# Performance work log

Measured on AMD Instinct MI355X. Metric: run time of the kernel, lower is better.

## Reference

```python
import jax, jax.numpy as jnp
import numpy as np

N_NODES = 50000
IN_F = 128
OUT_F = 128
N_EDGES = 800000
N_TRAIN = 5000


def setup_inputs() -> dict:
    key = jax.random.key(0)
    ks = jax.random.split(key, 7)
    x = jax.random.normal(ks[0], (N_NODES, IN_F), dtype=jnp.float32)
    edge_rows = jax.random.randint(ks[1], (N_EDGES,), 0, N_NODES)
    edge_cols = jax.random.randint(ks[2], (N_EDGES,), 0, N_NODES)
    adj_vals = jax.random.uniform(ks[3], (N_EDGES,), dtype=jnp.float32)
    train_fts_id = jax.random.randint(ks[4], (N_TRAIN,), 0, N_NODES)
    # xavier_uniform with gain sqrt(2)
    lim_W = np.sqrt(2.0) * np.sqrt(6.0 / (IN_F + OUT_F))
    W = jax.random.uniform(ks[5], (IN_F, OUT_F), dtype=jnp.float32, minval=-lim_W, maxval=lim_W)
    lim_M = np.sqrt(2.0) * np.sqrt(6.0 / (N_NODES + IN_F))
    M = jax.random.uniform(ks[6], (N_NODES, IN_F), dtype=jnp.float32, minval=-lim_M, maxval=lim_M)
    return {"x": x, "edge_rows": edge_rows, "edge_cols": edge_cols,
            "adj_vals": adj_vals, "train_fts_id": train_fts_id, "M": M, "W": W}


def reference(x, edge_rows, edge_cols, adj_vals, train_fts_id, M, W):
    n_nodes = M.shape[0]
    # M_eff = sigmoid(M), with rows at train_fts_id fixed to 1.0
    train_mask = jnp.zeros((n_nodes, 1), dtype=M.dtype).at[train_fts_id].set(1.0)
    M_eff = jnp.where(train_mask > 0, 1.0, jax.nn.sigmoid(M))  # [N, F]
    # AM = (non_norm_adj @ M_eff)^-1, inf -> 0 (binary non-normalized adjacency)
    denom = jax.ops.segment_sum(M_eff[edge_cols], edge_rows, num_segments=n_nodes)  # [N, F]
    AM = jnp.where(denom == 0, 0.0, 1.0 / jnp.where(denom == 0, 1.0, denom))
    # H = (sp_adj @ (M_eff * x)) * AM
    msg = adj_vals[:, None] * (M_eff * x)[edge_cols]  # [E, F]
    H = jax.ops.segment_sum(msg, edge_rows, num_segments=n_nodes) * AM  # [N, F]
    return jax.nn.elu(H @ W)  # [N, OUT_F]
```

## Files before the change

kernel.cpp:

```cpp
#include <hip/hip_runtime.h>
#include <hip/hip_fp16.h>

#define NN 50000
#define FF 128
#define NE 800000
#define NT 5000
#define NF (NN * FF)
#define NBKT 196
#define BCAP 8192
#define PADCOL 50000u
#define P1BLK 98
#define TRN_THREADS (NT * 32)

typedef __attribute__((ext_vector_type(8))) short bf16x8;
typedef __attribute__((ext_vector_type(4))) float f32x4;
typedef __attribute__((ext_vector_type(4))) unsigned u32x4;
typedef __attribute__((ext_vector_type(2))) unsigned u32x2;
typedef __attribute__((ext_vector_type(4))) int i32x4;

__device__ __forceinline__ unsigned bf16_rne(float f) {
    unsigned u = __float_as_uint(f);
    return (u + 0x7FFFu + ((u >> 16) & 1u)) >> 16;
}

__global__ void k_pack(const float* __restrict__ M, const float* __restrict__ x,
                       unsigned* __restrict__ Q, int* __restrict__ gcur) {
    int i4 = blockIdx.x * blockDim.x + threadIdx.x;
    if (i4 < 256) gcur[i4] = 0;
    if (i4 >= NF / 4 + FF / 4) return;
    u32x4* Q4 = reinterpret_cast<u32x4*>(Q);
    if (i4 >= NF / 4) {
        u32x4 z = {0, 0, 0, 0};
        Q4[i4] = z;
        return;
    }
    f32x4 m = __builtin_nontemporal_load(reinterpret_cast<const f32x4*>(M) + i4);
    f32x4 xv = __builtin_nontemporal_load(reinterpret_cast<const f32x4*>(x) + i4);
    float me0 = 1.0f / (1.0f + __expf(-m.x));
    float me1 = 1.0f / (1.0f + __expf(-m.y));
    float me2 = 1.0f / (1.0f + __expf(-m.z));
    float me3 = 1.0f / (1.0f + __expf(-m.w));
    u32x4 q;
    q.x = bf16_rne(me0) | (bf16_rne(me0 * xv.x) << 16);
    q.y = bf16_rne(me1) | (bf16_rne(me1 * xv.y) << 16);
    q.z = bf16_rne(me2) | (bf16_rne(me2 * xv.z) << 16);
    q.w = bf16_rne(me3) | (bf16_rne(me3 * xv.w) << 16);
    Q4[i4] = q;
}

__global__ __launch_bounds__(1024)
void k_pass1(const int* __restrict__ rows, const int* __restrict__ cols,
             const float* __restrict__ adj, const int* __restrict__ train,
             const float* __restrict__ x, unsigned* __restrict__ Q,
             int* __restrict__ gcur, unsigned long long* __restrict__ ebuf) {
    int t = threadIdx.x;
    if (blockIdx.x >= P1BLK) {
        int g = (blockIdx.x - P1BLK) * 1024 + t;
        if (g < TRN_THREADS) {
            int ti = g >> 5;
            int f4 = g & 31;
            int id = train[ti];
            f32x4 xv = reinterpret_cast<const f32x4*>(x)[id * 32 + f4];
            u32x4 q;
            q.x = 0x3F80u | (bf16_rne(xv.x) << 16);
            q.y = 0x3F80u | (bf16_rne(xv.y) << 16);
            q.z = 0x3F80u | (bf16_rne(xv.z) << 16);
            q.w = 0x3F80u | (bf16_rne(xv.w) << 16);
            reinterpret_cast<u32x4*>(Q)[id * 32 + f4] = q;
        }
        return;
    }
    __shared__ int hist[256];
    __shared__ int cur[256];
    if (t < 256) hist[t] = 0;
    __syncthreads();
    int base = blockIdx.x * 8192;
    int r[8], c[8], bkt[8];
    float a[8];
#pragma unroll
    for (int k = 0; k < 8; ++k) {
        int idx = base + k * 1024 + t;
        bool v = idx < NE;
        r[k] = v ? rows[idx] : 0;
        c[k] = v ? cols[idx] : 0;
        a[k] = v ? adj[idx] : 0.f;
        bkt[k] = v ? (r[k] >> 8) : -1;
        if (v) atomicAdd(&hist[bkt[k]], 1);
    }
    __syncthreads();
    if (t < 256) {
        int cnt = hist[t];
        int b = 0;
        if (cnt > 0) b = atomicAdd(&gcur[t], cnt);
        cur[t] = b;
    }
    __syncthreads();
#pragma unroll
    for (int k = 0; k < 8; ++k) {
        if (bkt[k] >= 0) {
            int p = atomicAdd(&cur[bkt[k]], 1);
            if (p < BCAP) {
                unsigned h = (unsigned)__half_as_ushort(__float2half_rn(a[k]));
                unsigned pk = (unsigned)c[k] | (h << 16);
                ebuf[(size_t)bkt[k] * BCAP + p] =
                    ((unsigned long long)(r[k] & 255) << 32) | pk;
            }
        }
    }
}

__global__ __launch_bounds__(1024)
void k_pass2(const int* __restrict__ gcur,
             const unsigned long long* __restrict__ ebuf,
             unsigned* __restrict__ gedges, int* __restrict__ offsets) {
    __shared__ int hist[256];
    __shared__ int scan[256];
    __shared__ int cur[256];
    __shared__ int bscan[256];
    int b = blockIdx.x;
    int t = threadIdx.x;
    if (t < 256) {
        bscan[t] = (t < NBKT) ? min(gcur[t], BCAP) : 0;
        hist[t] = 0;
    }
    __syncthreads();
    for (int d = 1; d < 256; d <<= 1) {
        int v = (t < 256 && t >= d) ? bscan[t - d] : 0;
        __syncthreads();
        if (t < 256) bscan[t] += v;
        __syncthreads();
    }
    int cnt = min(gcur[b], BCAP);
    int gstart = (b > 0) ? bscan[b - 1] : 0;
    const unsigned long long* eb = ebuf + (size_t)b * BCAP;
    unsigned long long rec[8];
#pragma unroll
    for (int k = 0; k < 8; ++k) {
        int idx = k * 1024 + t;
        rec[k] = 0;
        bool v = idx < cnt;
        if (v) {
            rec[k] = eb[idx];
            atomicAdd(&hist[(int)(rec[k] >> 32)], 1);
        }
    }
    __syncthreads();
    if (t < 256) scan[t] = hist[t];
    __syncthreads();
    for (int d = 1; d < 256; d <<= 1) {
        int v = (t < 256 && t >= d) ? scan[t - d] : 0;
        __syncthreads();
        if (t < 256) scan[t] += v;
        __syncthreads();
    }
    if (t < 256) {
        int excl = scan[t] - hist[t];
        cur[t] = excl;
        int row = b * 256 + t;
        if (row < NN) offsets[row] = gstart + excl;
    }
    if (b == NBKT - 1 && t == 0) offsets[NN] = gstart + cnt;
    __syncthreads();
#pragma unroll
    for (int k = 0; k < 8; ++k) {
        int idx = k * 1024 + t;
        if (idx < cnt) {
            int lr = (int)(rec[k] >> 32);
            int p = atomicAdd(&cur[lr], 1);
            gedges[gstart + p] = (unsigned)(rec[k] & 0xFFFFFFFFu);
        }
    }
}

__global__ __launch_bounds__(256)
void k_gather(const int* __restrict__ offsets, const unsigned* __restrict__ gedges,
              const unsigned* __restrict__ Q, unsigned* __restrict__ Hnb) {
    int t = blockIdx.x * blockDim.x + threadIdx.x;
    int wv = t >> 6;
    int lane = t & 63;
    int ra = wv * 2, rb = ra + 1;
    if (ra >= NN) return;
    int ba = offsets[ra];
    int bb = offsets[rb];
    int eb2 = offsets[rb + 1];
    int dega = bb - ba, degb = eb2 - bb;
    int nmax = (max(dega, degb) + 3) >> 2;
    const u32x2* Q2 = reinterpret_cast<const u32x2*>(Q);
    const unsigned padrec = PADCOL;
    float da0 = 0.f, da1 = 0.f, ha0 = 0.f, ha1 = 0.f;
    float db0 = 0.f, db1 = 0.f, hb0 = 0.f, hb1 = 0.f;
    for (int c = 0; c < nmax; ++c) {
        int ia = ba + c * 4, ib = bb + c * 4;
        unsigned ea[4], ebv[4];
#pragma unroll
        for (int i = 0; i < 4; ++i) {
            ea[i]  = (ia + i < bb)  ? gedges[ia + i] : padrec;
            ebv[i] = (ib + i < eb2) ? gedges[ib + i] : padrec;
        }
#pragma unroll
        for (int i = 0; i < 4; ++i) {
            unsigned ca = ea[i] & 0xFFFFu, cb = ebv[i] & 0xFFFFu;
            float aa = __half2float(__ushort_as_half((unsigned short)(ea[i] >> 16)));
            float ab = __half2float(__ushort_as_half((unsigned short)(ebv[i] >> 16)));
            u32x2 qa = Q2[(int)ca * 64 + lane];
            u32x2 qb = Q2[(int)cb * 64 + lane];
            da0 += __uint_as_float(qa.x << 16);
            da1 += __uint_as_float(qa.y << 16);
            ha0 += aa * __uint_as_float(qa.x & 0xFFFF0000u);
            ha1 += aa * __uint_as_float(qa.y & 0xFFFF0000u);
            db0 += __uint_as_float(qb.x << 16);
            db1 += __uint_as_float(qb.y << 16);
            hb0 += ab * __uint_as_float(qb.x & 0xFFFF0000u);
            hb1 += ab * __uint_as_float(qb.y & 0xFFFF0000u);
        }
    }
    float oa0 = (da0 == 0.f) ? 0.f : ha0 / da0;
    float oa1 = (da1 == 0.f) ? 0.f : ha1 / da1;
    float ob0 = (db0 == 0.f) ? 0.f : hb0 / db0;
    float ob1 = (db1 == 0.f) ? 0.f : hb1 / db1;
    Hnb[ra * 64 + lane] = bf16_rne(oa0) | (bf16_rne(oa1) << 16);
    Hnb[rb * 64 + lane] = bf16_rne(ob0) | (bf16_rne(ob1) << 16);
}

__global__ __launch_bounds__(256)
void k_gemm(const unsigned* __restrict__ Hnb, const float* __restrict__ W,
            float* __restrict__ out) {
    __shared__ short Wb[128 * 128];
    int tid = threadIdx.x;

#pragma unroll
    for (int i = 0; i < 8; ++i) {
        int c = tid + i * 256;
        int nl = c & 15;
        int t8 = (c >> 4) & 7;
        int ks = (c >> 7) & 3;
        int lh = (c >> 9) & 3;
        int l = nl | (lh << 4);
        int n = t8 * 16 + nl;
        int k0 = ks * 32 + lh * 8;
        short v[8];
#pragma unroll
        for (int j = 0; j < 8; ++j)
            v[j] = (short)bf16_rne(W[(k0 + j) * 128 + n]);
        *reinterpret_cast<bf16x8*>(&Wb[((t8 * 4 + ks) * 64 + l) * 8]) =
            *reinterpret_cast<bf16x8*>(v);
    }
    __syncthreads();

    int wave = tid >> 6, lane = tid & 63;
    int r0 = blockIdx.x * 64 + wave * 16;
    int mrow = lane & 15;
    int kg = lane >> 4;
    int arow = min(r0 + mrow, NN - 1);
    const u32x4* H4 = reinterpret_cast<const u32x4*>(Hnb);

    bf16x8 a[4];
#pragma unroll
    for (int ks = 0; ks < 4; ++ks) {
        u32x4 v = H4[(size_t)arow * 16 + ks * 4 + kg];
        a[ks] = *reinterpret_cast<bf16x8*>(&v);
    }

    f32x4 acc[8];
#pragma unroll
    for (int t8 = 0; t8 < 8; ++t8) acc[t8] = (f32x4){0.f, 0.f, 0.f, 0.f};

#pragma unroll
    for (int t8 = 0; t8 < 8; ++t8) {
#pragma unroll
        for (int ks = 0; ks < 4; ++ks) {
            bf16x8 b = *reinterpret_cast<const bf16x8*>(
                &Wb[((t8 * 4 + ks) * 64 + lane) * 8]);
            acc[t8] = __builtin_amdgcn_mfma_f32_16x16x32_bf16(a[ks], b, acc[t8], 0, 0, 0);
        }
    }

    int colb = lane & 15;
    int rsub = (lane >> 4) * 4;
#pragma unroll
    for (int t8 = 0; t8 < 8; ++t8) {
#pragma unroll
        for (int rg = 0; rg < 4; ++rg) {
            int row = r0 + rsub + rg;
            if (row < NN) {
                float v = acc[t8][rg];
                float o = (v > 0.f) ? v : (__expf(v) - 1.0f);
                __builtin_nontemporal_store(o, &out[(size_t)row * 128 + t8 * 16 + colb]);
            }
        }
    }
}

__global__ void k_init_fb(float* __restrict__ denomH, int* __restrict__ flags) {
    int i = blockIdx.x * blockDim.x + threadIdx.x;
    const int total4 = (2 * NF) / 4;
    if (i < total4)
        reinterpret_cast<float4*>(denomH)[i] = make_float4(0.f, 0.f, 0.f, 0.f);
    if (i < NN) flags[i] = 0;
}

__global__ void k_flags_fb(const int* __restrict__ ids, int* __restrict__ flags) {
    int i = blockIdx.x * blockDim.x + threadIdx.x;
    if (i < NT) flags[ids[i]] = 1;
}

__global__ __launch_bounds__(256)
void k_edge_fb(const int* __restrict__ rows, const int* __restrict__ cols,
               const float* __restrict__ adj, const float* __restrict__ M,
               const int* __restrict__ flags, const float* __restrict__ x,
               float* __restrict__ denom, float* __restrict__ H) {
    int t = blockIdx.x * blockDim.x + threadIdx.x;
    int e = t >> 6;
    int lane = t & 63;
    if (e >= NE) return;
    int r = rows[e], c = cols[e];
    float a = adj[e];
#pragma unroll
    for (int i = 0; i < 2; ++i) {
        int f = lane + i * 64;
        float m = M[c * FF + f];
        float me = flags[c] ? 1.0f : 1.0f / (1.0f + __expf(-m));
        float xv = x[c * FF + f];
        unsafeAtomicAdd(&denom[r * FF + f], me);
        unsafeAtomicAdd(&H[r * FF + f], a * me * xv);
    }
}

__global__ __launch_bounds__(256)
void k_norm_fb(const float* __restrict__ H, const float* __restrict__ denom,
               float* __restrict__ Hn) {
    int i = blockIdx.x * blockDim.x + threadIdx.x;
    if (i >= NF) return;
    float d = denom[i];
    Hn[i] = (d == 0.f) ? 0.f : H[i] / d;
}

__global__ __launch_bounds__(256)
void k_gemm_fb(const float* __restrict__ Hn, const float* __restrict__ W,
               float* __restrict__ out) {
    __shared__ float Ws[128][128];
    __shared__ float Hs[32][128];
    int tid = threadIdx.x;
    const float4* W4 = reinterpret_cast<const float4*>(W);
    float4* Ws4 = reinterpret_cast<float4*>(&Ws[0][0]);
#pragma unroll
    for (int i = 0; i < 16; ++i) Ws4[tid + i * 256] = W4[tid + i * 256];
    int r0 = blockIdx.x * 32;
    const float4* H4 = reinterpret_cast<const float4*>(Hn);
    float4* Hs4 = reinterpret_cast<float4*>(&Hs[0][0]);
#pragma unroll
    for (int i = 0; i < 4; ++i) {
        int m = tid + i * 256;
        int r = m >> 5, k4 = m & 31;
        int row = r0 + r;
        Hs4[m] = (row < NN) ? H4[row * 32 + k4] : make_float4(0.f, 0.f, 0.f, 0.f);
    }
    __syncthreads();
    int c = tid & 127, rg = tid >> 7;
    float acc[16];
#pragma unroll
    for (int i = 0; i < 16; ++i) acc[i] = 0.f;
    for (int k = 0; k < 128; k += 4) {
        float w0 = Ws[k][c], w1 = Ws[k + 1][c], w2 = Ws[k + 2][c], w3 = Ws[k + 3][c];
#pragma unroll
        for (int i = 0; i < 16; ++i) {
            float4 h = *reinterpret_cast<const float4*>(&Hs[rg * 16 + i][k]);
            acc[i] += h.x * w0 + h.y * w1 + h.z * w2 + h.w * w3;
        }
    }
#pragma unroll
    for (int i = 0; i < 16; ++i) {
        int row = r0 + rg * 16 + i;
        if (row < NN) {
            float v = acc[i];
            out[row * 128 + c] = (v > 0.f) ? v : (__expf(v) - 1.0f);
        }
    }
}

extern "C" void kernel_launch(void* const* d_in, const int* in_sizes, int n_in,
                              void* d_out, int out_size, void* d_ws, size_t ws_size,
                              hipStream_t stream) {
    const float* x     = (const float*)d_in[0];
    const int*   erows = (const int*)d_in[1];
    const int*   ecols = (const int*)d_in[2];
    const float* adj   = (const float*)d_in[3];
    const int*   train = (const int*)d_in[4];
    const float* M     = (const float*)d_in[5];
    const float* W     = (const float*)d_in[6];
    float* out = (float*)d_out;
    float* ws  = (float*)d_ws;

    const size_t UNI = ((size_t)NBKT * BCAP * 2 > (size_t)NF / 2)
                           ? (size_t)NBKT * BCAP * 2 : (size_t)NF / 2;
    size_t fo = 0;
    unsigned* Q   = (unsigned*)(ws + fo); fo += NF + FF;
    unsigned* Hnb = (unsigned*)(ws + fo);
    unsigned long long* ebuf = (unsigned long long*)(ws + fo); fo += UNI;
    unsigned* gedges = (unsigned*)(ws + fo); fo += NE;
    int* offsets  = (int*)(ws + fo); fo += NN + 1;
    int* gcur     = (int*)(ws + fo); fo += 256;
    const size_t need = fo * 4;

    if (ws_size >= need) {
        const int trn_blocks = (TRN_THREADS + 1023) / 1024;
        k_pack<<<(NF / 4 + FF / 4 + 255) / 256, 256, 0, stream>>>(M, x, Q, gcur);
        k_pass1<<<P1BLK + trn_blocks, 1024, 0, stream>>>(
            erows, ecols, adj, train, x, Q, gcur, ebuf);
        k_pass2<<<NBKT, 1024, 0, stream>>>(gcur, ebuf, gedges, offsets);
        k_gather<<<((NN / 2) * 64 + 255) / 256, 256, 0, stream>>>(offsets, gedges, Q, Hnb);
        k_gemm<<<(NN + 63) / 64, 256, 0, stream>>>(Hnb, W, out);
    } else {
        float* denom = ws;
        float* H     = ws + NF;
        int* flags_fb = (int*)(ws + 2 * (size_t)NF);
        k_init_fb<<<(2 * NF / 4 + 255) / 256, 256, 0, stream>>>(denom, flags_fb);
        k_flags_fb<<<(NT + 255) / 256, 256, 0, stream>>>(train, flags_fb);
        k_edge_fb<<<((size_t)NE * 64 + 255) / 256, 256, 0, stream>>>(
            erows, ecols, adj, M, flags_fb, x, denom, H);
        k_norm_fb<<<(NF + 255) / 256, 256, 0, stream>>>(H, denom, denom);
        k_gemm_fb<<<(NN + 31) / 32, 256, 0, stream>>>(denom, W, out);
    }
}
```

Before: 107.3 us.

## Co-schedule packing with edge bucketing and move train-row override into pass2

The elementwise sigmoid/bf16 packing of M and x moves out of its own kernel and runs as extra blocks of the edge-bucketing kernel, so the bandwidth-bound pack overlaps the atomic-heavy bucketing. The train-row overwrite moves into the pass2 kernel as extra blocks, which keeps it ordered after the pack. A tiny init kernel now zeroes the bucket counters. The gather loop also gets a fast path with unconditional edge loads for full chunks of four. This trades one launch for another and makes block scheduling between the two kinds of work less predictable.

```diff
diff --git a/kernel.cpp b/kernel.cpp
--- a/kernel.cpp
+++ b/kernel.cpp
@@ -10,7 +10,10 @@
 #define BCAP 8192
 #define PADCOL 50000u
 #define P1BLK 98
-#define TRN_THREADS (NT * 32)
+#define PACKN (NF / 4 + FF / 4)
+#define PACKB ((PACKN + 1023) / 1024)
+#define TRNN (NT * 32)
+#define TRNB ((TRNN + 1023) / 1024)
 
 typedef __attribute__((ext_vector_type(8))) short bf16x8;
 typedef __attribute__((ext_vector_type(4))) float f32x4;
@@ -23,40 +26,88 @@
     return (u + 0x7FFFu + ((u >> 16) & 1u)) >> 16;
 }
 
-__global__ void k_pack(const float* __restrict__ M, const float* __restrict__ x,
-                       unsigned* __restrict__ Q, int* __restrict__ gcur) {
-    int i4 = blockIdx.x * blockDim.x + threadIdx.x;
-    if (i4 < 256) gcur[i4] = 0;
-    if (i4 >= NF / 4 + FF / 4) return;
-    u32x4* Q4 = reinterpret_cast<u32x4*>(Q);
-    if (i4 >= NF / 4) {
-        u32x4 z = {0, 0, 0, 0};
-        Q4[i4] = z;
-        return;
-    }
-    f32x4 m = __builtin_nontemporal_load(reinterpret_cast<const f32x4*>(M) + i4);
-    f32x4 xv = __builtin_nontemporal_load(reinterpret_cast<const f32x4*>(x) + i4);
-    float me0 = 1.0f / (1.0f + __expf(-m.x));
-    float me1 = 1.0f / (1.0f + __expf(-m.y));
-    float me2 = 1.0f / (1.0f + __expf(-m.z));
-    float me3 = 1.0f / (1.0f + __expf(-m.w));
-    u32x4 q;
-    q.x = bf16_rne(me0) | (bf16_rne(me0 * xv.x) << 16);
-    q.y = bf16_rne(me1) | (bf16_rne(me1 * xv.y) << 16);
-    q.z = bf16_rne(me2) | (bf16_rne(me2 * xv.z) << 16);
-    q.w = bf16_rne(me3) | (bf16_rne(me3 * xv.w) << 16);
-    Q4[i4] = q;
+__global__ void k_init(int* __restrict__ gcur) {
+    if (threadIdx.x < 256) gcur[threadIdx.x] = 0;
 }
 
 __global__ __launch_bounds__(1024)
-void k_pass1(const int* __restrict__ rows, const int* __restrict__ cols,
-             const float* __restrict__ adj, const int* __restrict__ train,
-             const float* __restrict__ x, unsigned* __restrict__ Q,
-             int* __restrict__ gcur, unsigned long long* __restrict__ ebuf) {
+void k_sp(const int* __restrict__ rows, const int* __restrict__ cols,
+          const float* __restrict__ adj, const float* __restrict__ M,
+          const float* __restrict__ x, unsigned* __restrict__ Q,
+          int* __restrict__ gcur, unsigned long long* __restrict__ ebuf) {
     int t = threadIdx.x;
     if (blockIdx.x >= P1BLK) {
-        int g = (blockIdx.x - P1BLK) * 1024 + t;
-        if (g < TRN_THREADS) {
+        int i4 = (blockIdx.x - P1BLK) * 1024 + t;
+        if (i4 >= PACKN) return;
+        u32x4* Q4 = reinterpret_cast<u32x4*>(Q);
+        if (i4 >= NF / 4) {
+            u32x4 z = {0, 0, 0, 0};
+            Q4[i4] = z;
+            return;
+        }
+        f32x4 m = __builtin_nontemporal_load(reinterpret_cast<const f32x4*>(M) + i4);
+        f32x4 xv = __builtin_nontemporal_load(reinterpret_cast<const f32x4*>(x) + i4);
+        float me0 = 1.0f / (1.0f + __expf(-m.x));
+        float me1 = 1.0f / (1.0f + __expf(-m.y));
+        float me2 = 1.0f / (1.0f + __expf(-m.z));
+        float me3 = 1.0f / (1.0f + __expf(-m.w));
+        u32x4 q;
+        q.x = bf16_rne(me0) | (bf16_rne(me0 * xv.x) << 16);
+        q.y = bf16_rne(me1) | (bf16_rne(me1 * xv.y) << 16);
+        q.z = bf16_rne(me2) | (bf16_rne(me2 * xv.z) << 16);
+        q.w = bf16_rne(me3) | (bf16_rne(me3 * xv.w) << 16);
+        Q4[i4] = q;
+        return;
+    }
+    __shared__ int hist[256];
+    __shared__ int cur[256];
+    if (t < 256) hist[t] = 0;
+    __syncthreads();
+    int base = blockIdx.x * 8192;
+    int r[8], c[8], bkt[8];
+    float a[8];
+#pragma unroll
+    for (int k = 0; k < 8; ++k) {
+        int idx = base + k * 1024 + t;
+        bool v = idx < NE;
+        r[k] = v ? rows[idx] : 0;
+        c[k] = v ? cols[idx] : 0;
+        a[k] = v ? adj[idx] : 0.f;
+        bkt[k] = v ? (r[k] >> 8) : -1;
+        if (v) atomicAdd(&hist[bkt[k]], 1);
+    }
+    __syncthreads();
+    if (t < 256) {
+        int cnt = hist[t];
+        int b = 0;
+        if (cnt > 0) b = atomicAdd(&gcur[t], cnt);
+        cur[t] = b;
+    }
+    __syncthreads();
+#pragma unroll
+    for (int k = 0; k < 8; ++k) {
+        if (bkt[k] >= 0) {
+            int p = atomicAdd(&cur[bkt[k]], 1);
+            if (p < BCAP) {
+                unsigned h = (unsigned)__half_as_ushort(__float2half_rn(a[k]));
+                unsigned pk = (unsigned)c[k] | (h << 16);
+                ebuf[(size_t)bkt[k] * BCAP + p] =
+                    ((unsigned long long)(r[k] & 255) << 32) | pk;
+            }
+        }
+    }
+}
+
+__global__ __launch_bounds__(1024)
+void k_pass2(const int* __restrict__ gcur,
+             const unsigned long long* __restrict__ ebuf,
+             unsigned* __restrict__ gedges, int* __restrict__ offsets,
+             const int* __restrict__ train, const float* __restrict__ x,
+             unsigned* __restrict__ Q) {
+    int t = threadIdx.x;
+    if (blockIdx.x >= NBKT) {
+        int g = (blockIdx.x - NBKT) * 1024 + t;
+        if (g < TRNN) {
             int ti = g >> 5;
             int f4 = g & 31;
             int id = train[ti];
@@ -71,54 +122,10 @@
         return;
     }
     __shared__ int hist[256];
-    __shared__ int cur[256];
-    if (t < 256) hist[t] = 0;
-    __syncthreads();
-    int base = blockIdx.x * 8192;
-    int r[8], c[8], bkt[8];
-    float a[8];
-#pragma unroll
-    for (int k = 0; k < 8; ++k) {
-        int idx = base + k * 1024 + t;
-        bool v = idx < NE;
-        r[k] = v ? rows[idx] : 0;
-        c[k] = v ? cols[idx] : 0;
-        a[k] = v ? adj[idx] : 0.f;
-        bkt[k] = v ? (r[k] >> 8) : -1;
-        if (v) atomicAdd(&hist[bkt[k]], 1);
-    }
-    __syncthreads();
-    if (t < 256) {
-        int cnt = hist[t];
-        int b = 0;
-        if (cnt > 0) b = atomicAdd(&gcur[t], cnt);
-        cur[t] = b;
-    }
-    __syncthreads();
-#pragma unroll
-    for (int k = 0; k < 8; ++k) {
-        if (bkt[k] >= 0) {
-            int p = atomicAdd(&cur[bkt[k]], 1);
-            if (p < BCAP) {
-                unsigned h = (unsigned)__half_as_ushort(__float2half_rn(a[k]));
-                unsigned pk = (unsigned)c[k] | (h << 16);
-                ebuf[(size_t)bkt[k] * BCAP + p] =
-                    ((unsigned long long)(r[k] & 255) << 32) | pk;
-            }
-        }
-    }
-}
-
-__global__ __launch_bounds__(1024)
-void k_pass2(const int* __restrict__ gcur,
-             const unsigned long long* __restrict__ ebuf,
-             unsigned* __restrict__ gedges, int* __restrict__ offsets) {
-    __shared__ int hist[256];
     __shared__ int scan[256];
     __shared__ int cur[256];
     __shared__ int bscan[256];
     int b = blockIdx.x;
-    int t = threadIdx.x;
     if (t < 256) {
         bscan[t] = (t < NBKT) ? min(gcur[t], BCAP) : 0;
         hist[t] = 0;
@@ -138,8 +145,7 @@
     for (int k = 0; k < 8; ++k) {
         int idx = k * 1024 + t;
         rec[k] = 0;
-        bool v = idx < cnt;
-        if (v) {
+        if (idx < cnt) {
             rec[k] = eb[idx];
             atomicAdd(&hist[(int)(rec[k] >> 32)], 1);
         }
@@ -192,10 +198,21 @@
     for (int c = 0; c < nmax; ++c) {
         int ia = ba + c * 4, ib = bb + c * 4;
         unsigned ea[4], ebv[4];
-#pragma unroll
-        for (int i = 0; i < 4; ++i) {
-            ea[i]  = (ia + i < bb)  ? gedges[ia + i] : padrec;
-            ebv[i] = (ib + i < eb2) ? gedges[ib + i] : padrec;
+        if (ia + 4 <= bb) {
+#pragma unroll
+            for (int i = 0; i < 4; ++i) ea[i] = gedges[ia + i];
+        } else {
+#pragma unroll
+            for (int i = 0; i < 4; ++i)
+                ea[i] = (ia + i < bb) ? gedges[ia + i] : padrec;
+        }
+        if (ib + 4 <= eb2) {
+#pragma unroll
+            for (int i = 0; i < 4; ++i) ebv[i] = gedges[ib + i];
+        } else {
+#pragma unroll
+            for (int i = 0; i < 4; ++i)
+                ebv[i] = (ib + i < eb2) ? gedges[ib + i] : padrec;
         }
 #pragma unroll
         for (int i = 0; i < 4; ++i) {
@@ -403,11 +420,11 @@
     const size_t need = fo * 4;
 
     if (ws_size >= need) {
-        const int trn_blocks = (TRN_THREADS + 1023) / 1024;
-        k_pack<<<(NF / 4 + FF / 4 + 255) / 256, 256, 0, stream>>>(M, x, Q, gcur);
-        k_pass1<<<P1BLK + trn_blocks, 1024, 0, stream>>>(
-            erows, ecols, adj, train, x, Q, gcur, ebuf);
-        k_pass2<<<NBKT, 1024, 0, stream>>>(gcur, ebuf, gedges, offsets);
+        k_init<<<1, 256, 0, stream>>>(gcur);
+        k_sp<<<P1BLK + PACKB, 1024, 0, stream>>>(
+            erows, ecols, adj, M, x, Q, gcur, ebuf);
+        k_pass2<<<NBKT + TRNB, 1024, 0, stream>>>(
+            gcur, ebuf, gedges, offsets, train, x, Q);
         k_gather<<<((NN / 2) * 64 + 255) / 256, 256, 0, stream>>>(offsets, gedges, Q, Hnb);
         k_gemm<<<(NN + 63) / 64, 256, 0, stream>>>(Hnb, W, out);
     } else {
```

After: 109.2 us. No clear change (+1.8%).
